# Optimization experiments

Hardware: AMD Instinct MI355X
Metric: run time of the kernel (lower is better)

Reference implementation:

```python
import jax, jax.numpy as jnp
import numpy as np

EMBED = 1024
HEAD = 64

def setup_inputs() -> dict:
    key = jax.random.key(0)
    k1, k2, k3, k4 = jax.random.split(key, 4)
    # Torch Linear weight layout: [out_features, in_features]; xavier_uniform init
    bound = float(np.sqrt(6.0 / (EMBED + HEAD)))
    embeddings = jax.random.normal(k1, (4, 4096, EMBED), dtype=jnp.float32)
    W_Q = jax.random.uniform(k2, (HEAD, EMBED), dtype=jnp.float32, minval=-bound, maxval=bound)
    W_K = jax.random.uniform(k3, (HEAD, EMBED), dtype=jnp.float32, minval=-bound, maxval=bound)
    W_V = jax.random.uniform(k4, (HEAD, EMBED), dtype=jnp.float32, minval=-bound, maxval=bound)
    return {"embeddings": embeddings, "W_Q": W_Q, "W_K": W_K, "W_V": W_V}

def reference(embeddings, W_Q, W_K, W_V):
    # embeddings: [B, S, E]; weights: [H, E] (torch Linear layout, y = x @ W.T)
    B, S, E = embeddings.shape
    H = W_Q.shape[0]
    Q = jnp.einsum('bse,he->bsh', embeddings, W_Q)
    K = jnp.einsum('bse,he->bsh', embeddings, W_K)
    V = jnp.einsum('bse,he->bsh', embeddings, W_V)
    scale = 1.0 / jnp.sqrt(jnp.float32(H))
    scores = jnp.einsum('bqh,bkh->bqk', Q, K) * scale  # [B, S, S]
    causal = jnp.tril(jnp.ones((S, S), dtype=bool))
    scores = jnp.where(causal, scores, -jnp.inf)
    attn = jax.nn.softmax(scores, axis=-1)
    # dropout (p=0.1) is identity at inference; omitted for determinism
    return jnp.einsum('bqk,bkh->bqh', attn, V)  # [B, S, H]
```

## Files before the change

### kernel.cpp

```cpp
#include <hip/hip_runtime.h>
#include <hip/hip_bf16.h>

#define EMBED 1024
#define SEQ   4096
#define NBATCH 4
#define HD    64
#define CH    8
#define NP    8

typedef __attribute__((ext_vector_type(8))) short s16x8;
typedef __attribute__((ext_vector_type(4))) float f32x4;
typedef __attribute__((ext_vector_type(4))) unsigned int u32x4;

__device__ __forceinline__ short f2bf(float f) {
    unsigned u = __builtin_bit_cast(unsigned, f);
    u += 0x7fffu + ((u >> 16) & 1u);
    return (short)(u >> 16);
}
__device__ __forceinline__ float bf2f(short h) {
    unsigned u = ((unsigned)(unsigned short)h) << 16;
    return __builtin_bit_cast(float, u);
}

typedef const unsigned int __attribute__((address_space(1)))* gbl_ptr_t;
typedef unsigned int __attribute__((address_space(3)))* lds_ptr_t;
__device__ __forceinline__ void async16(const void* g, void* l) {
    __builtin_amdgcn_global_load_lds((gbl_ptr_t)g, (lds_ptr_t)l, 16, 0, 0);
}

__global__ __launch_bounds__(256) void prep_w(
    const float* __restrict__ wq, const float* __restrict__ wk,
    const float* __restrict__ wv, short* __restrict__ Wb)
{
    int idx = blockIdx.x * 256 + threadIdx.x;
    int e = idx * 8;
    int row = e >> 10, col = e & 1023;
    const float* src = (row < 64) ? (wq + (size_t)row * EMBED)
                     : (row < 128) ? (wk + (size_t)(row - 64) * EMBED)
                                   : (wv + (size_t)(row - 128) * EMBED);
    float sc = (row < 64) ? 0.125f : 1.0f;
    float4 f0 = *(const float4*)(src + col);
    float4 f1 = *(const float4*)(src + col + 4);
    s16x8 v = { f2bf(f0.x*sc), f2bf(f0.y*sc), f2bf(f0.z*sc), f2bf(f0.w*sc),
                f2bf(f1.x*sc), f2bf(f1.y*sc), f2bf(f1.z*sc), f2bf(f1.w*sc) };
    *(s16x8*)&Wb[e] = v;
}

__global__ __launch_bounds__(512) void proj_qkv(
    const float* __restrict__ emb, const short* __restrict__ Wb,
    short* __restrict__ Qb, short* __restrict__ Kb, short* __restrict__ Vt)
{
    __shared__ short Alds[2][64 * 64];
    __shared__ short Blds[2][192 * 64];

    const int tid  = threadIdx.x;
    const int lane = tid & 63;
    const int w    = tid >> 6;
    const int wr   = w & 3;
    const int wc   = w >> 2;
    const int row0 = blockIdx.x * 64;
    const int l15  = lane & 15;
    const int g    = lane >> 4;

    const int sr   = tid >> 3;
    const int sg   = tid & 7;
    const int srow = lane >> 3;
    const int sblk = lane & 7;

    f32x4 acc[6];
#pragma unroll
    for (int i = 0; i < 6; ++i) acc[i] = f32x4{0.f, 0.f, 0.f, 0.f};

    auto stageB = [&](int buf, int t) {
        const int k0 = t * 64;
#pragma unroll
        for (int i = 0; i < 3; ++i) {
            int r = w * 24 + i * 8 + srow;
            async16(Wb + (size_t)r * EMBED + k0 + ((sblk ^ (r & 7)) * 8),
                    &Blds[buf][(w * 24 + i * 8) * 64]);
        }
    };
    const float* abase = emb + (size_t)(row0 + sr) * EMBED + sg * 8;
    auto writeA = [&](int buf, float4 f0, float4 f1) {
        s16x8 v = { f2bf(f0.x), f2bf(f0.y), f2bf(f0.z), f2bf(f0.w),
                    f2bf(f1.x), f2bf(f1.y), f2bf(f1.z), f2bf(f1.w) };
        *(s16x8*)&Alds[buf][sr * 64 + ((sg ^ (sr & 7)) * 8)] = v;
    };

    float4 f0a = *(const float4*)(abase);
    float4 f1a = *(const float4*)(abase + 4);
    stageB(0, 0);
    writeA(0, f0a, f1a);
    f0a = *(const float4*)(abase + 64);
    f1a = *(const float4*)(abase + 68);
    __syncthreads();

    int cur = 0;
    const int ar = wr * 16 + l15;
    float4 f0b = f0a, f1b = f1a;

    for (int t = 0; t < 16; ++t) {
        if (t < 14) {
            f0b = *(const float4*)(abase + (size_t)(t + 2) * 64);
            f1b = *(const float4*)(abase + (size_t)(t + 2) * 64 + 4);
        }
        if (t < 15) stageB(cur ^ 1, t + 1);

        s16x8 a0 = *(const s16x8*)&Alds[cur][ar * 64 + (((g    ) ^ (ar & 7)) * 8)];
        s16x8 a1 = *(const s16x8*)&Alds[cur][ar * 64 + (((g + 4) ^ (ar & 7)) * 8)];
#pragma unroll
        for (int n = 0; n < 6; ++n) {
            int br = wc * 96 + n * 16 + l15;
            s16x8 b0 = *(const s16x8*)&Blds[cur][br * 64 + (((g    ) ^ (br & 7)) * 8)];
            s16x8 b1 = *(const s16x8*)&Blds[cur][br * 64 + (((g + 4) ^ (br & 7)) * 8)];
            acc[n] = __builtin_amdgcn_mfma_f32_16x16x32_bf16(a0, b0, acc[n], 0, 0, 0);
            acc[n] = __builtin_amdgcn_mfma_f32_16x16x32_bf16(a1, b1, acc[n], 0, 0, 0);
        }
        if (t < 15) writeA(cur ^ 1, f0a, f1a);
        __syncthreads();
        f0a = f0b; f1a = f1b;
        cur ^= 1;
    }

    const int rbase = row0 + wr * 16 + g * 4;
#pragma unroll
    for (int n = 0; n < 6; ++n) {
        int col = wc * 96 + n * 16 + l15;
        int mat = col >> 6;
        int c = col & 63;
#pragma unroll
        for (int r = 0; r < 4; ++r) {
            int row = rbase + r;
            int b = row >> 12, s = row & 4095;
            short v = f2bf(acc[n][r]);
            if (mat == 0)       Qb[((size_t)b * SEQ + s) * HD + c] = v;
            else if (mat == 1)  Kb[((size_t)b * SEQ + s) * HD + c] = v;
            else                Vt[((size_t)b * HD + c) * SEQ + s] = v;
        }
    }
}

__global__ __launch_bounds__(256) void attn_fwd(
    const short* __restrict__ Qb, const short* __restrict__ Kb,
    const short* __restrict__ Vt, float* __restrict__ Op, float* __restrict__ Ml)
{
    const int jq = blockIdx.x;
    const int b  = blockIdx.y;
    const int p  = blockIdx.z;
    const int t0 = p * CH;
    if (t0 > jq) return;
    const int t1 = min(t0 + CH, jq + 1);

    __shared__ short Qlds[64 * 64];
    __shared__ short Klds[2][64 * 64];
    __shared__ short Vlds[2][64 * 64];

    const int tid  = threadIdx.x;
    const int lane = tid & 63;
    const int w    = tid >> 6;
    const int l15  = lane & 15;
    const int g    = lane >> 4;
    const int q0w  = jq * 64 + w * 16;

    const short* Qbase  = Qb + ((size_t)b * SEQ + jq * 64) * HD;
    const short* Kbase0 = Kb + (size_t)b * SEQ * HD;
    const short* Vbase0 = Vt + (size_t)b * HD * SEQ;

    const int srow = lane >> 3;
    const int sblk = lane & 7;

    auto stageKV = [&](int buf, int t) {
        const int kv0 = t * 64;
#pragma unroll
        for (int i = 0; i < 2; ++i) {
            int r = w * 16 + i * 8 + srow;
            async16(Kbase0 + (size_t)(kv0 + r) * HD + ((sblk ^ (r & 7)) * 8),
                    &Klds[buf][(w * 16 + i * 8) * 64]);
            async16(Vbase0 + (size_t)r * SEQ + kv0 + ((sblk ^ (r & 7)) * 8),
                    &Vlds[buf][(w * 16 + i * 8) * 64]);
        }
    };

#pragma unroll
    for (int i = 0; i < 2; ++i) {
        int r = w * 16 + i * 8 + srow;
        async16(Qbase + (size_t)r * HD + ((sblk ^ (r & 7)) * 8),
                &Qlds[(w * 16 + i * 8) * 64]);
    }
    stageKV(0, t0);
    __syncthreads();

    const int qr = w * 16 + l15;
    s16x8 qb0 = *(const s16x8*)&Qlds[qr * 64 + (((g    ) ^ (qr & 7)) * 8)];
    s16x8 qb1 = *(const s16x8*)&Qlds[qr * 64 + (((g + 4) ^ (qr & 7)) * 8)];

    f32x4 o[4];
#pragma unroll
    for (int n = 0; n < 4; ++n) o[n] = f32x4{0.f, 0.f, 0.f, 0.f};
    float m = -INFINITY, l = 0.f;

    const int f1l = (2 * (g & 1) + (g >> 1)) * 16 + l15;
    const int f2l = (2 * (g & 1) + 1 - (g >> 1)) * 16 + l15;
    const bool podd = (g & 1) != 0;
    const bool hbit = (g >> 1) != 0;

    int cur = 0;
    for (int t = t0; t < t1; ++t) {
        if (t + 1 < t1) stageKV(cur ^ 1, t + 1);

        f32x4 st[4];
#pragma unroll
        for (int n = 0; n < 4; ++n) {
            int kr = n * 16 + l15;
            s16x8 ka0 = *(const s16x8*)&Klds[cur][kr * 64 + (((g    ) ^ (kr & 7)) * 8)];
            s16x8 ka1 = *(const s16x8*)&Klds[cur][kr * 64 + (((g + 4) ^ (kr & 7)) * 8)];
            st[n] = __builtin_amdgcn_mfma_f32_16x16x32_bf16(ka0, qb0, f32x4{0.f,0.f,0.f,0.f}, 0, 0, 0);
            st[n] = __builtin_amdgcn_mfma_f32_16x16x32_bf16(ka1, qb1, st[n], 0, 0, 0);
        }

        if (t == jq) {
#pragma unroll
            for (int n = 0; n < 4; ++n)
#pragma unroll
                for (int r = 0; r < 4; ++r) {
                    int kvg = t * 64 + n * 16 + g * 4 + r;
                    if (kvg > q0w + l15) st[n][r] = -INFINITY;
                }
        }

        float mt = fmaxf(fmaxf(st[0][0], st[0][1]), fmaxf(st[0][2], st[0][3]));
#pragma unroll
        for (int n = 1; n < 4; ++n)
            mt = fmaxf(mt, fmaxf(fmaxf(st[n][0], st[n][1]), fmaxf(st[n][2], st[n][3])));
        mt = fmaxf(mt, __shfl_xor(mt, 16, 64));
        mt = fmaxf(mt, __shfl_xor(mt, 32, 64));

        float mn  = fmaxf(m, mt);
        float fac = __expf(m - mn);
        m = mn;

        float rs = 0.f;
        unsigned pk[4][2];
#pragma unroll
        for (int n = 0; n < 4; ++n) {
            unsigned u0 = (unsigned)(unsigned short)f2bf(__expf(st[n][0] - m));
            unsigned u1 = (unsigned)(unsigned short)f2bf(__expf(st[n][1] - m));
            unsigned u2 = (unsigned)(unsigned short)f2bf(__expf(st[n][2] - m));
            unsigned u3 = (unsigned)(unsigned short)f2bf(__expf(st[n][3] - m));
            pk[n][0] = u0 | (u1 << 16);
            pk[n][1] = u2 | (u3 << 16);
            rs += bf2f((short)u0) + bf2f((short)u1) + bf2f((short)u2) + bf2f((short)u3);
        }
        rs += __shfl_xor(rs, 16, 64);
        rs += __shfl_xor(rs, 32, 64);
        l = l * fac + rs;
#pragma unroll
        for (int n = 0; n < 4; ++n)
#pragma unroll
            for (int r = 0; r < 4; ++r) o[n][r] *= fac;

#pragma unroll
        for (int kk = 0; kk < 2; ++kk) {
            unsigned e00 = podd ? pk[2 * kk + 1][0] : pk[2 * kk][0];
            unsigned e01 = podd ? pk[2 * kk + 1][1] : pk[2 * kk][1];
            unsigned e10 = podd ? pk[2 * kk][0]     : pk[2 * kk + 1][0];
            unsigned e11 = podd ? pk[2 * kk][1]     : pk[2 * kk + 1][1];
            unsigned x0 = (unsigned)__shfl((int)e00, f1l, 64);
            unsigned x1 = (unsigned)__shfl((int)e01, f1l, 64);
            unsigned y0 = (unsigned)__shfl((int)e10, f2l, 64);
            unsigned y1 = (unsigned)__shfl((int)e11, f2l, 64);
            unsigned w0 = hbit ? y0 : x0;
            unsigned w1 = hbit ? y1 : x1;
            unsigned w2 = hbit ? x0 : y0;
            unsigned w3 = hbit ? x1 : y1;
            u32x4 uu = { w0, w1, w2, w3 };
            s16x8 pb = __builtin_bit_cast(s16x8, uu);
#pragma unroll
            for (int n = 0; n < 4; ++n) {
                int vr = n * 16 + l15;
                s16x8 va = *(const s16x8*)&Vlds[cur][vr * 64 + (((g + kk * 4) ^ (vr & 7)) * 8)];
                o[n] = __builtin_amdgcn_mfma_f32_16x16x32_bf16(va, pb, o[n], 0, 0, 0);
            }
        }
        __syncthreads();
        cur ^= 1;
    }

    const size_t pidx = ((size_t)b * 64 + jq) * NP + p;
    float* opb = Op + pidx * 4096;
#pragma unroll
    for (int n = 0; n < 4; ++n)
#pragma unroll
        for (int r = 0; r < 4; ++r)
            opb[(n * 16 + g * 4 + r) * 64 + w * 16 + l15] = o[n][r];
    if (lane < 16) {
        float* mlb = Ml + pidx * 128;
        mlb[w * 16 + l15]      = m;
        mlb[64 + w * 16 + l15] = l;
    }
}

__global__ __launch_bounds__(256) void attn_combine(
    const float* __restrict__ Op, const float* __restrict__ Ml,
    float* __restrict__ out)
{
    const int jq = blockIdx.x;
    const int b  = blockIdx.y;
    const int nP = (jq >> 3) + 1;
    const int tid = threadIdx.x;
    const int q  = tid & 63;
    const int dc = tid >> 6;
    const size_t pb = ((size_t)b * 64 + jq) * NP;

    float mv[NP], lv[NP], wt[NP];
    float mstar = -INFINITY;
#pragma unroll
    for (int p = 0; p < NP; ++p) if (p < nP) {
        mv[p] = Ml[(pb + p) * 128 + q];
        lv[p] = Ml[(pb + p) * 128 + 64 + q];
        mstar = fmaxf(mstar, mv[p]);
    }
    float L = 0.f;
#pragma unroll
    for (int p = 0; p < NP; ++p) if (p < nP) {
        wt[p] = __expf(mv[p] - mstar);
        L += lv[p] * wt[p];
    }
    float inv = 1.0f / L;

    float acc[16];
#pragma unroll
    for (int k = 0; k < 16; ++k) acc[k] = 0.f;
#pragma unroll
    for (int p = 0; p < NP; ++p) if (p < nP) {
        const float* src = Op + (pb + p) * 4096 + (size_t)dc * 16 * 64 + q;
#pragma unroll
        for (int k = 0; k < 16; ++k) acc[k] += src[k * 64] * wt[p];
    }
    float* dst = out + ((size_t)b * SEQ + jq * 64 + q) * HD + dc * 16;
#pragma unroll
    for (int k = 0; k < 16; ++k) dst[k] = acc[k] * inv;
}

extern "C" void kernel_launch(void* const* d_in, const int* in_sizes, int n_in,
                              void* d_out, int out_size, void* d_ws, size_t ws_size,
                              hipStream_t stream)
{
    (void)in_sizes; (void)n_in; (void)out_size; (void)ws_size;
    const float* emb = (const float*)d_in[0];
    const float* wq  = (const float*)d_in[1];
    const float* wk  = (const float*)d_in[2];
    const float* wv  = (const float*)d_in[3];
    float* out = (float*)d_out;

    short* Wb = (short*)d_ws;
    short* Qb = Wb + 192 * 1024;
    short* Kb = Qb + (size_t)NBATCH * SEQ * HD;
    short* Vt = Kb + (size_t)NBATCH * SEQ * HD;
    float* Op = (float*)(Vt + (size_t)NBATCH * SEQ * HD);
    float* Ml = Op + (size_t)NBATCH * 64 * NP * 64 * 64;

    hipLaunchKernelGGL(prep_w, dim3(96), dim3(256), 0, stream, wq, wk, wv, Wb);
    hipLaunchKernelGGL(proj_qkv, dim3(256), dim3(512), 0, stream, emb, Wb, Qb, Kb, Vt);
    hipLaunchKernelGGL(attn_fwd, dim3(64, NBATCH, NP), dim3(256), 0, stream,
                       Qb, Kb, Vt, Op, Ml);
    hipLaunchKernelGGL(attn_combine, dim3(64, NBATCH), dim3(256), 0, stream,
                       Op, Ml, out);
}
```

Measured before the change: 154.7 us.

## Retile projection, reorder attention grid, add lazy rescale and packed bf16 convert

The projection kernel now uses 32-row tiles with 256 threads across 512 blocks, doubling the grid to spread work over more CUs. The attention grid is reordered so the heaviest query tiles launch first, and MFMA sections get raised wave priority. Online-softmax rescaling is skipped unless the running max grows by more than 8, and probabilities are packed with a hardware bf16 convert instruction. The row sum now uses unrounded fp32 values, which differ slightly from the bf16 values fed to the PV product.

After: 150.7 us. 1.03x faster.

```diff
diff --git a/kernel.cpp b/kernel.cpp
--- a/kernel.cpp
+++ b/kernel.cpp
@@ -16,10 +16,6 @@
     unsigned u = __builtin_bit_cast(unsigned, f);
     u += 0x7fffu + ((u >> 16) & 1u);
     return (short)(u >> 16);
-}
-__device__ __forceinline__ float bf2f(short h) {
-    unsigned u = ((unsigned)(unsigned short)h) << 16;
-    return __builtin_bit_cast(float, u);
 }
 
 typedef const unsigned int __attribute__((address_space(1)))* gbl_ptr_t;
@@ -46,21 +42,19 @@
     *(s16x8*)&Wb[e] = v;
 }
 
-__global__ __launch_bounds__(512) void proj_qkv(
+__global__ __launch_bounds__(256) void proj_qkv(
     const float* __restrict__ emb, const short* __restrict__ Wb,
     short* __restrict__ Qb, short* __restrict__ Kb, short* __restrict__ Vt)
 {
-    __shared__ short Alds[2][64 * 64];
+    __shared__ short Alds[2][32 * 64];
     __shared__ short Blds[2][192 * 64];
 
     const int tid  = threadIdx.x;
     const int lane = tid & 63;
     const int w    = tid >> 6;
-    const int wr   = w & 3;
-    const int wc   = w >> 2;
-    const int row0 = blockIdx.x * 64;
-    const int l15  = lane & 15;
-    const int g    = lane >> 4;
+    const int wr   = w & 1;
+    const int wc   = w >> 1;
+    const int row0 = blockIdx.x * 32;
 
     const int sr   = tid >> 3;
     const int sg   = tid & 7;
@@ -74,10 +68,10 @@
     auto stageB = [&](int buf, int t) {
         const int k0 = t * 64;
 #pragma unroll
-        for (int i = 0; i < 3; ++i) {
-            int r = w * 24 + i * 8 + srow;
+        for (int i = 0; i < 6; ++i) {
+            int r = w * 48 + i * 8 + srow;
             async16(Wb + (size_t)r * EMBED + k0 + ((sblk ^ (r & 7)) * 8),
-                    &Blds[buf][(w * 24 + i * 8) * 64]);
+                    &Blds[buf][(w * 48 + i * 8) * 64]);
         }
     };
     const float* abase = emb + (size_t)(row0 + sr) * EMBED + sg * 8;
@@ -96,7 +90,8 @@
     __syncthreads();
 
     int cur = 0;
-    const int ar = wr * 16 + l15;
+    const int ar = wr * 16 + (lane & 15);
+    const int ag = lane >> 4;
     float4 f0b = f0a, f1b = f1a;
 
     for (int t = 0; t < 16; ++t) {
@@ -106,13 +101,13 @@
         }
         if (t < 15) stageB(cur ^ 1, t + 1);
 
-        s16x8 a0 = *(const s16x8*)&Alds[cur][ar * 64 + (((g    ) ^ (ar & 7)) * 8)];
-        s16x8 a1 = *(const s16x8*)&Alds[cur][ar * 64 + (((g + 4) ^ (ar & 7)) * 8)];
+        s16x8 a0 = *(const s16x8*)&Alds[cur][ar * 64 + (((ag    ) ^ (ar & 7)) * 8)];
+        s16x8 a1 = *(const s16x8*)&Alds[cur][ar * 64 + (((ag + 4) ^ (ar & 7)) * 8)];
 #pragma unroll
         for (int n = 0; n < 6; ++n) {
-            int br = wc * 96 + n * 16 + l15;
-            s16x8 b0 = *(const s16x8*)&Blds[cur][br * 64 + (((g    ) ^ (br & 7)) * 8)];
-            s16x8 b1 = *(const s16x8*)&Blds[cur][br * 64 + (((g + 4) ^ (br & 7)) * 8)];
+            int br = wc * 96 + n * 16 + (lane & 15);
+            s16x8 b0 = *(const s16x8*)&Blds[cur][br * 64 + (((ag    ) ^ (br & 7)) * 8)];
+            s16x8 b1 = *(const s16x8*)&Blds[cur][br * 64 + (((ag + 4) ^ (br & 7)) * 8)];
             acc[n] = __builtin_amdgcn_mfma_f32_16x16x32_bf16(a0, b0, acc[n], 0, 0, 0);
             acc[n] = __builtin_amdgcn_mfma_f32_16x16x32_bf16(a1, b1, acc[n], 0, 0, 0);
         }
@@ -122,10 +117,11 @@
         cur ^= 1;
     }
 
-    const int rbase = row0 + wr * 16 + g * 4;
+    const int rbase = row0 + wr * 16 + ((lane >> 4) * 4);
+    const int cl = lane & 15;
 #pragma unroll
     for (int n = 0; n < 6; ++n) {
-        int col = wc * 96 + n * 16 + l15;
+        int col = wc * 96 + n * 16 + cl;
         int mat = col >> 6;
         int c = col & 63;
 #pragma unroll
@@ -144,9 +140,9 @@
     const short* __restrict__ Qb, const short* __restrict__ Kb,
     const short* __restrict__ Vt, float* __restrict__ Op, float* __restrict__ Ml)
 {
-    const int jq = blockIdx.x;
-    const int b  = blockIdx.y;
-    const int p  = blockIdx.z;
+    const int jq = 63 - blockIdx.x;
+    const int b  = blockIdx.z;
+    const int p  = blockIdx.y;
     const int t0 = p * CH;
     if (t0 > jq) return;
     const int t1 = min(t0 + CH, jq + 1);
@@ -209,6 +205,7 @@
         if (t + 1 < t1) stageKV(cur ^ 1, t + 1);
 
         f32x4 st[4];
+        __builtin_amdgcn_s_setprio(1);
 #pragma unroll
         for (int n = 0; n < 4; ++n) {
             int kr = n * 16 + l15;
@@ -217,6 +214,7 @@
             st[n] = __builtin_amdgcn_mfma_f32_16x16x32_bf16(ka0, qb0, f32x4{0.f,0.f,0.f,0.f}, 0, 0, 0);
             st[n] = __builtin_amdgcn_mfma_f32_16x16x32_bf16(ka1, qb1, st[n], 0, 0, 0);
         }
+        __builtin_amdgcn_s_setprio(0);
 
         if (t == jq) {
 #pragma unroll
@@ -235,30 +233,34 @@
         mt = fmaxf(mt, __shfl_xor(mt, 16, 64));
         mt = fmaxf(mt, __shfl_xor(mt, 32, 64));
 
-        float mn  = fmaxf(m, mt);
-        float fac = __expf(m - mn);
-        m = mn;
+        if (__any(mt - m > 8.f)) {
+            float mn  = fmaxf(m, mt);
+            float fac = __expf(m - mn);
+            m = mn;
+            l *= fac;
+#pragma unroll
+            for (int n = 0; n < 4; ++n)
+#pragma unroll
+                for (int r = 0; r < 4; ++r) o[n][r] *= fac;
+        }
 
         float rs = 0.f;
         unsigned pk[4][2];
 #pragma unroll
         for (int n = 0; n < 4; ++n) {
-            unsigned u0 = (unsigned)(unsigned short)f2bf(__expf(st[n][0] - m));
-            unsigned u1 = (unsigned)(unsigned short)f2bf(__expf(st[n][1] - m));
-            unsigned u2 = (unsigned)(unsigned short)f2bf(__expf(st[n][2] - m));
-            unsigned u3 = (unsigned)(unsigned short)f2bf(__expf(st[n][3] - m));
-            pk[n][0] = u0 | (u1 << 16);
-            pk[n][1] = u2 | (u3 << 16);
-            rs += bf2f((short)u0) + bf2f((short)u1) + bf2f((short)u2) + bf2f((short)u3);
+            float p0 = __expf(st[n][0] - m);
+            float p1 = __expf(st[n][1] - m);
+            float p2 = __expf(st[n][2] - m);
+            float p3 = __expf(st[n][3] - m);
+            rs += (p0 + p1) + (p2 + p3);
+            asm("v_cvt_pk_bf16_f32 %0, %1, %2" : "=v"(pk[n][0]) : "v"(p0), "v"(p1));
+            asm("v_cvt_pk_bf16_f32 %0, %1, %2" : "=v"(pk[n][1]) : "v"(p2), "v"(p3));
         }
         rs += __shfl_xor(rs, 16, 64);
         rs += __shfl_xor(rs, 32, 64);
-        l = l * fac + rs;
-#pragma unroll
-        for (int n = 0; n < 4; ++n)
-#pragma unroll
-            for (int r = 0; r < 4; ++r) o[n][r] *= fac;
-
+        l += rs;
+
+        __builtin_amdgcn_s_setprio(1);
 #pragma unroll
         for (int kk = 0; kk < 2; ++kk) {
             unsigned e00 = podd ? pk[2 * kk + 1][0] : pk[2 * kk][0];
@@ -282,6 +284,7 @@
                 o[n] = __builtin_amdgcn_mfma_f32_16x16x32_bf16(va, pb, o[n], 0, 0, 0);
             }
         }
+        __builtin_amdgcn_s_setprio(0);
         __syncthreads();
         cur ^= 1;
     }
@@ -361,8 +364,8 @@
     float* Ml = Op + (size_t)NBATCH * 64 * NP * 64 * 64;
 
     hipLaunchKernelGGL(prep_w, dim3(96), dim3(256), 0, stream, wq, wk, wv, Wb);
-    hipLaunchKernelGGL(proj_qkv, dim3(256), dim3(512), 0, stream, emb, Wb, Qb, Kb, Vt);
-    hipLaunchKernelGGL(attn_fwd, dim3(64, NBATCH, NP), dim3(256), 0, stream,
+    hipLaunchKernelGGL(proj_qkv, dim3(512), dim3(256), 0, stream, emb, Wb, Qb, Kb, Vt);
+    hipLaunchKernelGGL(attn_fwd, dim3(64, NP, NBATCH), dim3(256), 0, stream,
                        Qb, Kb, Vt, Op, Ml);
     hipLaunchKernelGGL(attn_combine, dim3(64, NBATCH), dim3(256), 0, stream,
                        Op, Ml, out);
```
